# Kernel optimization log

Hardware: AMD Instinct MI355X
Metric: run time of the kernel (lower is better)

## Reference

```python
import jax, jax.numpy as jnp
import numpy as np

V, E, H, TAG, L = 50000, 256, 256, 20, 2
T = TAG + 2  # +START/STOP
START, STOP = TAG, TAG + 1
B, S = 128, 256
EPS = 1e-5


def _lstm_dir(x, w_ih, w_hh, b_ih, b_hh, reverse):
    # x: [B,S,in]; w_ih: [4H,in]; w_hh: [4H,H]
    xg = jnp.einsum('bsi,gi->bsg', x, w_ih) + b_ih  # [B,S,4H]
    Hd = w_hh.shape[-1]
    def step(carry, xt):
        h, c = carry
        g = xt + h @ w_hh.T + b_hh
        i, f, gg, o = jnp.split(g, 4, axis=-1)  # torch gate order i,f,g,o
        c = jax.nn.sigmoid(f) * c + jax.nn.sigmoid(i) * jnp.tanh(gg)
        h = jax.nn.sigmoid(o) * jnp.tanh(c)
        return (h, c), h
    init = (jnp.zeros((x.shape[0], Hd), x.dtype), jnp.zeros((x.shape[0], Hd), x.dtype))
    _, hs = jax.lax.scan(step, init, xg.transpose(1, 0, 2), reverse=reverse)
    return hs.transpose(1, 0, 2)


def _bilstm_layer(x, w_ih, w_hh, b_ih, b_hh):
    fwd = _lstm_dir(x, w_ih[0], w_hh[0], b_ih[0], b_hh[0], False)
    bwd = _lstm_dir(x, w_ih[1], w_hh[1], b_ih[1], b_hh[1], True)
    return jnp.concatenate([fwd, bwd], axis=-1)


def _crf_nll(feats, mask, tags, trans):
    # feats: [B,S,T]; trans[from,to]; mask: [B,S] int
    Bn, Sn, Tn = feats.shape
    m = mask.astype(feats.dtype)
    # --- log partition via forward algorithm ---
    alpha = trans[START][None, :] + feats[:, 0]  # [B,T]
    def step(alpha, inp):
        emit, mt = inp  # [B,T], [B]
        new = jax.nn.logsumexp(alpha[:, :, None] + trans[None, :, :], axis=1) + emit
        return jnp.where(mt[:, None] > 0, new, alpha), None
    alpha, _ = jax.lax.scan(step, alpha, (feats[:, 1:].transpose(1, 0, 2), mask[:, 1:].T))
    logZ = jax.nn.logsumexp(alpha + trans[:, STOP][None, :], axis=1)  # [B]
    # --- gold path score ---
    emit = jnp.take_along_axis(feats, tags[:, :, None], axis=2)[:, :, 0]  # [B,S]
    emit_score = (emit * m).sum(axis=1)
    tr_score = trans[START, tags[:, 0]]
    tr_score = tr_score + (trans[tags[:, :-1], tags[:, 1:]] * m[:, 1:]).sum(axis=1)
    last_idx = (mask.sum(axis=1) - 1).astype(jnp.int32)
    last_tag = jnp.take_along_axis(tags, last_idx[:, None].astype(tags.dtype), axis=1)[:, 0]
    tr_score = tr_score + trans[last_tag, STOP]
    return jnp.mean(logZ - emit_score - tr_score)


def _forward(embedding, w_ih0, w_hh0, b_ih0, b_hh0, w_ih1, w_hh1, b_ih1, b_hh1,
             ln_g, ln_b, w_out, b_out, trans, word_input, mask, tags):
    x = embedding[word_input]  # [B,S,E] (dropout off at eval)
    x = _bilstm_layer(x, w_ih0, w_hh0, b_ih0, b_hh0)  # [B,S,2H]
    x = _bilstm_layer(x, w_ih1, w_hh1, b_ih1, b_hh1)  # [B,S,2H]
    mu = x.mean(axis=-1, keepdims=True)
    var = ((x - mu) ** 2).mean(axis=-1, keepdims=True)
    x = (x - mu) * jax.lax.rsqrt(var + EPS) * ln_g + ln_b
    feats = jnp.einsum('bsh,th->bst', x, w_out) + b_out  # [B,S,T]
    return _crf_nll(feats, mask, tags, trans)


def setup_inputs() -> dict:
    key = jax.random.key(0)
    ks = jax.random.split(key, 20)
    sc = 0.05
    inp = {
        'embedding': jax.random.uniform(ks[0], (V, E), jnp.float32, -0.1, 0.1),
        'w_ih0': jax.random.normal(ks[1], (2, 4 * H, E), jnp.float32) * sc,
        'w_hh0': jax.random.normal(ks[2], (2, 4 * H, H), jnp.float32) * sc,
        'b_ih0': jnp.zeros((2, 4 * H), jnp.float32),
        'b_hh0': jnp.zeros((2, 4 * H), jnp.float32),
        'w_ih1': jax.random.normal(ks[3], (2, 4 * H, 2 * H), jnp.float32) * sc,
        'w_hh1': jax.random.normal(ks[4], (2, 4 * H, H), jnp.float32) * sc,
        'b_ih1': jnp.zeros((2, 4 * H), jnp.float32),
        'b_hh1': jnp.zeros((2, 4 * H), jnp.float32),
        'ln_g': jnp.ones((2 * H,), jnp.float32),
        'ln_b': jnp.zeros((2 * H,), jnp.float32),
        'w_out': jax.random.normal(ks[5], (T, 2 * H), jnp.float32) * sc,
        'b_out': jnp.zeros((T,), jnp.float32),
        'trans': jax.random.normal(ks[6], (T, T), jnp.float32) * sc,
        'word_input': jax.random.randint(ks[7], (B, S), 0, V, jnp.int64),
        'mask': jnp.ones((B, S), jnp.int32),
        'tags': jax.random.randint(ks[8], (B, S), 0, TAG, jnp.int64),
    }
    return inp


def reference(embedding, w_ih0, w_hh0, b_ih0, b_hh0, w_ih1, w_hh1, b_ih1, b_hh1,
              ln_g, ln_b, w_out, b_out, trans, word_input, mask, tags):
    return _forward(embedding, w_ih0, w_hh0, b_ih0, b_hh0, w_ih1, w_hh1, b_ih1, b_hh1,
                    ln_g, ln_b, w_out, b_out, trans, word_input, mask, tags)
```

## Files before the change

kernel.cpp:

```cpp
#include <hip/hip_runtime.h>
#include <stdint.h>

#define DEVINL __device__ __forceinline__

typedef __attribute__((ext_vector_type(8))) __bf16 bf16x8;
typedef __attribute__((ext_vector_type(8))) unsigned short ushort8;
typedef __attribute__((ext_vector_type(4))) float floatx4;

constexpr int E_ = 256;
constexpr int TAGS = 22, ST_START = 20, ST_STOP = 21;
constexpr int B_ = 128, S_ = 256, BS_ = B_ * S_;
constexpr int NG = 1024;

DEVINL uint16_t f2bf(float f) {
  uint32_t u = __builtin_bit_cast(uint32_t, f);
  return (uint16_t)((u + 0x7fffu + ((u >> 16) & 1u)) >> 16);
}
DEVINL float bf2f(uint16_t h) {
  uint32_t u = ((uint32_t)h) << 16;
  return __builtin_bit_cast(float, u);
}
DEVINL uint4 pack8(float4 a, float4 b) {
  ushort8 h;
  h[0] = f2bf(a.x); h[1] = f2bf(a.y); h[2] = f2bf(a.z); h[3] = f2bf(a.w);
  h[4] = f2bf(b.x); h[5] = f2bf(b.y); h[6] = f2bf(b.z); h[7] = f2bf(b.w);
  return __builtin_bit_cast(uint4, h);
}
DEVINL floatx4 mfma16(uint4 a, uint4 b, floatx4 c) {
  return __builtin_amdgcn_mfma_f32_16x16x32_bf16(
      __builtin_bit_cast(bf16x8, a), __builtin_bit_cast(bf16x8, b), c, 0, 0, 0);
}
DEVINL float sigf(float x) { return 1.f / (1.f + __expf(-x)); }
DEVINL float tanh_(float x) { return 1.f - 2.f / (__expf(2.f * x) + 1.f); }

__global__ void k_init(float* out, int out_n) {
  int t = threadIdx.x;
  if (t < out_n) out[t] = 0.f;
}

__global__ void k_f2bf(const float* __restrict__ src, uint16_t* __restrict__ dst, int n) {
  int i = blockIdx.x * blockDim.x + threadIdx.x;
  int stride = gridDim.x * blockDim.x;
  for (; i < n; i += stride) dst[i] = f2bf(src[i]);
}

template <bool EMBED, int K>
__global__ __launch_bounds__(256) void k_gemm(
    const float* __restrict__ emb, const int* __restrict__ word,
    const uint16_t* __restrict__ xa, const uint16_t* __restrict__ wb,
    uint16_t* __restrict__ xg) {
  __shared__ uint4 As[8 * 128];
  __shared__ uint4 Bs[8 * 128];
  const int tid = threadIdx.x;
  const int bx = blockIdx.x;
  const int m0 = (bx & 255) << 7;
  const int n0 = (bx >> 8) << 7;
  const int lane = tid & 63, w = tid >> 6;
  const int ln = lane & 15, q = lane >> 4;
  const int wm = w & 1, wn = w >> 1;

  floatx4 acc[4][4];
#pragma unroll
  for (int a = 0; a < 4; a++)
#pragma unroll
    for (int b = 0; b < 4; b++) acc[a][b] = (floatx4){0.f, 0.f, 0.f, 0.f};

  for (int k0 = 0; k0 < K; k0 += 64) {
#pragma unroll
    for (int it = 0; it < 4; it++) {
      int c = tid + it * 256;
      int k8 = c & 7, r = c >> 3;
      if (EMBED) {
        int row = word[m0 + r];
        const float* sp = emb + (size_t)row * E_ + k0 + k8 * 8;
        float4 f0 = *(const float4*)sp;
        float4 f1 = *(const float4*)(sp + 4);
        As[k8 * 128 + r] = pack8(f0, f1);
      } else {
        As[k8 * 128 + r] = *(const uint4*)(xa + (size_t)(m0 + r) * K + k0 + k8 * 8);
      }
      Bs[k8 * 128 + r] = *(const uint4*)(wb + (size_t)(n0 + r) * K + k0 + k8 * 8);
    }
    __syncthreads();
#pragma unroll
    for (int kk = 0; kk < 2; kk++) {
      const int k4b = kk * 4 + q;
      uint4 af[4], bf[4];
#pragma unroll
      for (int mt = 0; mt < 4; mt++) af[mt] = As[k4b * 128 + wm * 64 + mt * 16 + ln];
#pragma unroll
      for (int nt = 0; nt < 4; nt++) bf[nt] = Bs[k4b * 128 + wn * 64 + nt * 16 + ln];
#pragma unroll
      for (int mt = 0; mt < 4; mt++)
#pragma unroll
        for (int nt = 0; nt < 4; nt++) acc[mt][nt] = mfma16(af[mt], bf[nt], acc[mt][nt]);
    }
    __syncthreads();
  }
#pragma unroll
  for (int mt = 0; mt < 4; mt++) {
    int Rb = m0 + wm * 64 + mt * 16 + q * 4;
#pragma unroll
    for (int nt = 0; nt < 4; nt++) {
      int C = n0 + wn * 64 + nt * 16 + ln;
      size_t base = (size_t)(C >> 10) * ((size_t)BS_ * NG) + (C & 1023);
#pragma unroll
      for (int r = 0; r < 4; r++) xg[base + (size_t)(Rb + r) * NG] = f2bf(acc[mt][nt][r]);
    }
  }
}

__global__ __launch_bounds__(256) void k_rec(
    const uint16_t* __restrict__ xg, const float* __restrict__ w_hh,
    const float* __restrict__ b_ih, const float* __restrict__ b_hh,
    uint16_t* __restrict__ xout, uint64_t* __restrict__ hbuf, int ebase) {
  __shared__ uint4 Wl[32 * 64];
  __shared__ uint32_t hA32[4096];
  __shared__ float gates[32 * 66];
  __shared__ uint32_t xstage[16 * 256];
  __shared__ float bias_s[64];

  const int tid = threadIdx.x;
  const int wg = blockIdx.x;
  const int group = wg & 7, member = wg >> 3;
  const int dir = group & 1, tile = group >> 1;
  const int j0 = member * 16;
  const int lane = tid & 63, w = tid >> 6, ln = lane & 15, q = lane >> 4;

  for (int p = tid; p < 2048; p += 256) {
    int n = p & 63, k4 = p >> 6;
    int row = dir * 1024 + (n >> 4) * 256 + j0 + (n & 15);
    const float* sp = w_hh + (size_t)row * 256 + k4 * 8;
    float4 f0 = *(const float4*)sp;
    float4 f1 = *(const float4*)(sp + 4);
    Wl[k4 * 64 + n] = pack8(f0, f1);
  }
  if (tid < 64) {
    int row = dir * 1024 + (tid >> 4) * 256 + j0 + (tid & 15);
    bias_s[tid] = b_ih[row] + b_hh[row];
  }
  __syncthreads();

  const int nloc = w * 16 + ln;
  const int nglob = w * 256 + j0 + ln;
  const float breg = bias_s[nloc];
  const uint16_t* xgd = xg + (size_t)dir * BS_ * NG;

  const int msr = tid & 31, jp = tid >> 5;
  const int cp = member * 8 + jp;
  const int e_pub = (cp >> 2) * 128 + msr * 4 + (cp & 3);
  float c0 = 0.f, c1 = 0.f;

  const int xr0 = tile * 32 + q * 4;
  int sg = dir ? 255 : 0;
  uint16_t xv[8];
#pragma unroll
  for (int r = 0; r < 4; r++) {
    xv[r] = xgd[(size_t)((xr0 + r) * 256 + sg) * NG + nglob];
    xv[4 + r] = xgd[(size_t)((xr0 + 16 + r) * 256 + sg) * NG + nglob];
  }

  const uint4* hAv = (const uint4*)hA32;

  for (int t = 0; t < 256; t++) {
    sg = dir ? (255 - t) : t;
    floatx4 acc0 = (floatx4){0.f, 0.f, 0.f, 0.f};
    floatx4 acc1 = (floatx4){0.f, 0.f, 0.f, 0.f};
    if (t > 0) {
      const uint64_t* hsrc = hbuf + (size_t)((((t - 1) & 1) * 8) + group) * 4096;
      const uint32_t want = (uint32_t)(ebase + t);
      uint64_t v[16];
      while (true) {
#pragma unroll
        for (int i = 0; i < 16; i++)
          v[i] = __hip_atomic_load(&hsrc[tid + 256 * i], __ATOMIC_RELAXED,
                                   __HIP_MEMORY_SCOPE_AGENT);
        bool fresh = true;
#pragma unroll
        for (int i = 0; i < 16; i++) fresh &= ((uint32_t)(v[i] >> 32) == want);
        if (fresh) break;
        __builtin_amdgcn_s_sleep(1);
      }
#pragma unroll
      for (int i = 0; i < 16; i++) hA32[tid + 256 * i] = (uint32_t)v[i];
      __syncthreads();
#pragma unroll
      for (int kk = 0; kk < 8; kk++) {
        int k4b = kk * 4 + q;
        uint4 bfr = Wl[k4b * 64 + nloc];
        acc0 = mfma16(hAv[k4b * 32 + ln], bfr, acc0);
        acc1 = mfma16(hAv[k4b * 32 + 16 + ln], bfr, acc1);
      }
    }
#pragma unroll
    for (int r = 0; r < 4; r++) {
      gates[(q * 4 + r) * 66 + nloc] = acc0[r] + bf2f(xv[r]) + breg;
      gates[(16 + q * 4 + r) * 66 + nloc] = acc1[r] + bf2f(xv[4 + r]) + breg;
    }
    {
      int tn = (t < 255) ? (t + 1) : 255;
      int sgn = dir ? (255 - tn) : tn;
#pragma unroll
      for (int r = 0; r < 4; r++) {
        xv[r] = xgd[(size_t)((xr0 + r) * 256 + sgn) * NG + nglob];
        xv[4 + r] = xgd[(size_t)((xr0 + 16 + r) * 256 + sgn) * NG + nglob];
      }
    }
    __syncthreads();
    const float* gr = gates + msr * 66 + 2 * jp;
    float ig0 = gr[0], fg0 = gr[16], gg0 = gr[32], og0 = gr[48];
    float ig1 = gr[1], fg1 = gr[17], gg1 = gr[33], og1 = gr[49];
    c0 = sigf(fg0) * c0 + sigf(ig0) * tanh_(gg0);
    c1 = sigf(fg1) * c1 + sigf(ig1) * tanh_(gg1);
    float h0 = sigf(og0) * tanh_(c0);
    float h1 = sigf(og1) * tanh_(c1);
    uint32_t hpack = (uint32_t)f2bf(h0) | ((uint32_t)f2bf(h1) << 16);
    xstage[(t & 15) * 256 + jp * 32 + msr] = hpack;
    if (t < 255) {
      uint64_t pk = (uint64_t)hpack | ((uint64_t)(uint32_t)(ebase + t + 1) << 32);
      __hip_atomic_store(&hbuf[(size_t)(((t & 1) * 8) + group) * 4096 + e_pub], pk,
                         __ATOMIC_RELAXED, __HIP_MEMORY_SCOPE_AGENT);
    }
    if ((t & 15) == 15) {
      __syncthreads();
#pragma unroll
      for (int pp = 0; pp < 2; pp++) {
        int p = tid + pp * 256;
        int m = p & 31, u = p >> 5;
        int tt = t - 15 + u;
        int ssg = dir ? (255 - tt) : tt;
        uint32_t d[8];
#pragma unroll
        for (int jj = 0; jj < 8; jj++) d[jj] = xstage[u * 256 + jj * 32 + m];
        uint16_t* dst = xout + ((size_t)(tile * 32 + m) * 256 + ssg) * 512 + dir * 256 + j0;
        ((uint4*)dst)[0] = (uint4){d[0], d[1], d[2], d[3]};
        ((uint4*)dst)[1] = (uint4){d[4], d[5], d[6], d[7]};
      }
    }
  }
}

__global__ __launch_bounds__(256) void k_lnproj(
    const uint16_t* __restrict__ x2, const float* __restrict__ ln_g,
    const float* __restrict__ ln_b, const float* __restrict__ w_out,
    const float* __restrict__ b_out, float* __restrict__ feats) {
  const int w = threadIdx.x >> 6, lane = threadIdx.x & 63;
  const int row = blockIdx.x * 4 + w;
  ushort8 xu = __builtin_bit_cast(ushort8, *((const uint4*)(x2 + (size_t)row * 512) + lane));
  float f[8];
  float s = 0.f, ss = 0.f;
#pragma unroll
  for (int j = 0; j < 8; j++) {
    f[j] = bf2f(xu[j]);
    s += f[j];
    ss += f[j] * f[j];
  }
#pragma unroll
  for (int o = 1; o < 64; o <<= 1) {
    s += __shfl_xor(s, o, 64);
    ss += __shfl_xor(ss, o, 64);
  }
  float mu = s * (1.f / 512.f);
  float var = ss * (1.f / 512.f) - mu * mu;
  float rs = rsqrtf(var + 1e-5f);
  const float4 g0 = *(const float4*)(ln_g + lane * 8);
  const float4 g1 = *(const float4*)(ln_g + lane * 8 + 4);
  const float4 bb0 = *(const float4*)(ln_b + lane * 8);
  const float4 bb1 = *(const float4*)(ln_b + lane * 8 + 4);
  float gl[8] = {g0.x, g0.y, g0.z, g0.w, g1.x, g1.y, g1.z, g1.w};
  float bl[8] = {bb0.x, bb0.y, bb0.z, bb0.w, bb1.x, bb1.y, bb1.z, bb1.w};
  float xh[8];
#pragma unroll
  for (int j = 0; j < 8; j++) xh[j] = (f[j] - mu) * rs * gl[j] + bl[j];
  float* fr = feats + (size_t)row * TAGS;
  for (int tg = 0; tg < TAGS; tg++) {
    const float4 w0 = *(const float4*)(w_out + tg * 512 + lane * 8);
    const float4 w1 = *(const float4*)(w_out + tg * 512 + lane * 8 + 4);
    float p = xh[0] * w0.x + xh[1] * w0.y + xh[2] * w0.z + xh[3] * w0.w + xh[4] * w1.x +
              xh[5] * w1.y + xh[6] * w1.z + xh[7] * w1.w;
#pragma unroll
    for (int o = 1; o < 64; o <<= 1) p += __shfl_xor(p, o, 64);
    if (lane == 0) fr[tg] = p + b_out[tg];
  }
}

__global__ __launch_bounds__(64) void k_crf(
    const float* __restrict__ feats, const float* __restrict__ trans,
    const int* __restrict__ mask, const int* __restrict__ tags, float* __restrict__ out) {
  const int b = blockIdx.x, j = threadIdx.x;
  const bool act = j < TAGS;
  float tcol[TAGS];
#pragma unroll
  for (int i = 0; i < TAGS; i++) tcol[i] = act ? trans[i * TAGS + j] : 0.f;
  const float tstop = act ? trans[j * TAGS + ST_STOP] : 0.f;
  const float* fb = feats + (size_t)b * 256 * TAGS;
  const int* mb = mask + b * 256;
  const int* tb = tags + b * 256;
  float alpha = act ? (tcol[ST_START] + fb[j]) : -1e30f;
  for (int t = 1; t < 256; t++) {
    float vv[TAGS];
    float mx = -1e30f;
#pragma unroll
    for (int i = 0; i < TAGS; i++) {
      float v = __shfl(alpha, i, 64) + tcol[i];
      vv[i] = v;
      mx = fmaxf(mx, v);
    }
    float s = 0.f;
#pragma unroll
    for (int i = 0; i < TAGS; i++) s += __expf(vv[i] - mx);
    float nw = mx + __logf(s) + (act ? fb[t * TAGS + j] : 0.f);
    if (act && mb[t] > 0) alpha = nw;
  }
  float z = act ? (alpha + tstop) : -1e30f;
  float mz = z;
#pragma unroll
  for (int o = 1; o < 64; o <<= 1) mz = fmaxf(mz, __shfl_xor(mz, o, 64));
  float se = act ? __expf(z - mz) : 0.f;
#pragma unroll
  for (int o = 1; o < 64; o <<= 1) se += __shfl_xor(se, o, 64);
  float logZ = mz + __logf(se);
  float em = 0.f;
  int cnt = 0;
  for (int tt = j; tt < 256; tt += 64) {
    int m = mb[tt];
    cnt += m;
    if (m > 0) em += fb[tt * TAGS + tb[tt]];
  }
#pragma unroll
  for (int o = 1; o < 64; o <<= 1) {
    em += __shfl_xor(em, o, 64);
    cnt += __shfl_xor(cnt, o, 64);
  }
  float tr = 0.f;
  for (int tt = 1 + j; tt < 256; tt += 64)
    if (mb[tt] > 0) tr += trans[tb[tt - 1] * TAGS + tb[tt]];
#pragma unroll
  for (int o = 1; o < 64; o <<= 1) tr += __shfl_xor(tr, o, 64);
  if (j == 0) {
    tr += trans[ST_START * TAGS + tb[0]];
    int last = cnt - 1;
    tr += trans[tb[last] * TAGS + ST_STOP];
    atomicAdd(out, (logZ - em - tr) * (1.f / 128.f));
  }
}

extern "C" void kernel_launch(void* const* d_in, const int* in_sizes, int n_in, void* d_out,
                              int out_size, void* d_ws, size_t ws_size, hipStream_t stream) {
  (void)in_sizes;
  (void)n_in;
  const float* emb = (const float*)d_in[0];
  const float* w_ih0 = (const float*)d_in[1];
  const float* w_hh0 = (const float*)d_in[2];
  const float* b_ih0 = (const float*)d_in[3];
  const float* b_hh0 = (const float*)d_in[4];
  const float* w_ih1 = (const float*)d_in[5];
  const float* w_hh1 = (const float*)d_in[6];
  const float* b_ih1 = (const float*)d_in[7];
  const float* b_hh1 = (const float*)d_in[8];
  const float* ln_g = (const float*)d_in[9];
  const float* ln_b = (const float*)d_in[10];
  const float* w_out = (const float*)d_in[11];
  const float* b_out = (const float*)d_in[12];
  const float* trans = (const float*)d_in[13];
  const int* word = (const int*)d_in[14];
  const int* mask = (const int*)d_in[15];
  const int* tags = (const int*)d_in[16];

  char* ws = (char*)d_ws;
  size_t off = 0;
  auto take = [&](size_t bytes) -> char* {
    char* p = ws + off;
    off = (off + bytes + 255) & ~(size_t)255;
    return p;
  };
  uint16_t* wb0 = (uint16_t*)take((size_t)2048 * 256 * 2);
  uint16_t* wb1 = (uint16_t*)take((size_t)2048 * 512 * 2);
  uint16_t* xg = (uint16_t*)take((size_t)2 * BS_ * 1024 * 2);
  uint16_t* x1 = (uint16_t*)take((size_t)BS_ * 512 * 2);
  float* feats = (float*)take((size_t)BS_ * TAGS * 4);
  uint64_t* hbuf = (uint64_t*)take((size_t)2 * 8 * 4096 * 8);
  if (off > ws_size) return;
  float* out = (float*)d_out;

  hipLaunchKernelGGL(k_init, dim3(1), dim3(256), 0, stream, out, out_size);
  hipLaunchKernelGGL(k_f2bf, dim3(512), dim3(256), 0, stream, w_ih0, wb0, 2048 * 256);
  hipLaunchKernelGGL(k_f2bf, dim3(512), dim3(256), 0, stream, w_ih1, wb1, 2048 * 512);
  hipLaunchKernelGGL((k_gemm<true, 256>), dim3(4096), dim3(256), 0, stream, emb, word,
                     (const uint16_t*)nullptr, wb0, xg);
  hipLaunchKernelGGL(k_rec, dim3(128), dim3(256), 0, stream, xg, w_hh0, b_ih0, b_hh0, x1, hbuf,
                     0);
  hipLaunchKernelGGL((k_gemm<false, 512>), dim3(4096), dim3(256), 0, stream,
                     (const float*)nullptr, (const int*)nullptr, x1, wb1, xg);
  hipLaunchKernelGGL(k_rec, dim3(128), dim3(256), 0, stream, xg, w_hh1, b_ih1, b_hh1, x1, hbuf,
                     256);
  hipLaunchKernelGGL(k_lnproj, dim3(8192), dim3(256), 0, stream, x1, ln_g, ln_b, w_out, b_out,
                     feats);
  hipLaunchKernelGGL(k_crf, dim3(128), dim3(64), 0, stream, feats, trans, mask, tags, out);
}
```

Baseline: 1.671 ms.

## Halve recurrent workgroups, keep W_hh in registers, fuse gate math in-lane

The recurrent LSTM kernel now runs 64 workgroups that each own 32 hidden units instead of 128 owning 16. The W_hh slice is preloaded into registers, so the per-step MFMA loop no longer reads weights from LDS. Each lane computes all four gates for its own rows, which removes the gates LDS round-trip and one barrier per step. The h exchange buffer is double-buffered and output staging is flushed every 8 steps. The trade-off is fewer workgroups doing twice the work per step, much higher register pressure, and a longer spin-wait sleep.

```diff
diff --git a/kernel.cpp b/kernel.cpp
--- a/kernel.cpp
+++ b/kernel.cpp
@@ -110,62 +110,64 @@
   }
 }
 
-__global__ __launch_bounds__(256) void k_rec(
+__global__ __launch_bounds__(256, 1) void k_rec(
     const uint16_t* __restrict__ xg, const float* __restrict__ w_hh,
     const float* __restrict__ b_ih, const float* __restrict__ b_hh,
     uint16_t* __restrict__ xout, uint64_t* __restrict__ hbuf, int ebase) {
-  __shared__ uint4 Wl[32 * 64];
-  __shared__ uint32_t hA32[4096];
-  __shared__ float gates[32 * 66];
-  __shared__ uint32_t xstage[16 * 256];
-  __shared__ float bias_s[64];
+  __shared__ uint4 Wl[32 * 128];
+  __shared__ uint32_t hA32[2 * 4096];
+  __shared__ uint32_t xstage[8 * 512];
 
   const int tid = threadIdx.x;
   const int wg = blockIdx.x;
   const int group = wg & 7, member = wg >> 3;
   const int dir = group & 1, tile = group >> 1;
-  const int j0 = member * 16;
+  const int j0m = member * 32;
   const int lane = tid & 63, w = tid >> 6, ln = lane & 15, q = lane >> 4;
-
-  for (int p = tid; p < 2048; p += 256) {
-    int n = p & 63, k4 = p >> 6;
-    int row = dir * 1024 + (n >> 4) * 256 + j0 + (n & 15);
+  const int mh = w >> 1, jh = w & 1;
+
+  for (int p = tid; p < 4096; p += 256) {
+    int nloc = p & 127, k4 = p >> 7;
+    int g = (nloc >> 4) & 3, jj = (nloc >> 6) * 16 + (nloc & 15);
+    int row = dir * 1024 + g * 256 + j0m + jj;
     const float* sp = w_hh + (size_t)row * 256 + k4 * 8;
-    float4 f0 = *(const float4*)sp;
-    float4 f1 = *(const float4*)(sp + 4);
-    Wl[k4 * 64 + n] = pack8(f0, f1);
-  }
-  if (tid < 64) {
-    int row = dir * 1024 + (tid >> 4) * 256 + j0 + (tid & 15);
-    bias_s[tid] = b_ih[row] + b_hh[row];
-  }
+    Wl[k4 * 128 + nloc] = pack8(*(const float4*)sp, *(const float4*)(sp + 4));
+  }
+  const int j = j0m + jh * 16 + ln;
+  float brg[4];
+#pragma unroll
+  for (int g = 0; g < 4; g++) brg[g] = b_ih[dir * 1024 + g * 256 + j] +
+                                       b_hh[dir * 1024 + g * 256 + j];
   __syncthreads();
 
-  const int nloc = w * 16 + ln;
-  const int nglob = w * 256 + j0 + ln;
-  const float breg = bias_s[nloc];
+  uint4 Wb[8][4];
+#pragma unroll
+  for (int kk = 0; kk < 8; kk++)
+#pragma unroll
+    for (int g = 0; g < 4; g++)
+      Wb[kk][g] = Wl[(kk * 4 + q) * 128 + jh * 64 + g * 16 + ln];
+
   const uint16_t* xgd = xg + (size_t)dir * BS_ * NG;
-
-  const int msr = tid & 31, jp = tid >> 5;
-  const int cp = member * 8 + jp;
-  const int e_pub = (cp >> 2) * 128 + msr * 4 + (cp & 3);
-  float c0 = 0.f, c1 = 0.f;
-
-  const int xr0 = tile * 32 + q * 4;
+  const int mbase = mh * 16 + q * 4;
+  const int mrow0 = tile * 32 + mbase;
+  const bool even = (ln & 1) == 0;
+  const int jp = j >> 1;
+  const int jpl = jh * 8 + (ln >> 1);
+
+  float c[4] = {0.f, 0.f, 0.f, 0.f};
+  uint16_t xv[16];
   int sg = dir ? 255 : 0;
-  uint16_t xv[8];
-#pragma unroll
-  for (int r = 0; r < 4; r++) {
-    xv[r] = xgd[(size_t)((xr0 + r) * 256 + sg) * NG + nglob];
-    xv[4 + r] = xgd[(size_t)((xr0 + 16 + r) * 256 + sg) * NG + nglob];
-  }
-
-  const uint4* hAv = (const uint4*)hA32;
+#pragma unroll
+  for (int g = 0; g < 4; g++)
+#pragma unroll
+    for (int r = 0; r < 4; r++)
+      xv[g * 4 + r] = xgd[(size_t)((mrow0 + r) * 256 + sg) * NG + g * 256 + j];
 
   for (int t = 0; t < 256; t++) {
     sg = dir ? (255 - t) : t;
-    floatx4 acc0 = (floatx4){0.f, 0.f, 0.f, 0.f};
-    floatx4 acc1 = (floatx4){0.f, 0.f, 0.f, 0.f};
+    floatx4 acc[4];
+#pragma unroll
+    for (int g = 0; g < 4; g++) acc[g] = (floatx4){0.f, 0.f, 0.f, 0.f};
     if (t > 0) {
       const uint64_t* hsrc = hbuf + (size_t)((((t - 1) & 1) * 8) + group) * 4096;
       const uint32_t want = (uint32_t)(ebase + t);
@@ -179,63 +181,73 @@
 #pragma unroll
         for (int i = 0; i < 16; i++) fresh &= ((uint32_t)(v[i] >> 32) == want);
         if (fresh) break;
-        __builtin_amdgcn_s_sleep(1);
+        __builtin_amdgcn_s_sleep(2);
       }
-#pragma unroll
-      for (int i = 0; i < 16; i++) hA32[tid + 256 * i] = (uint32_t)v[i];
+      uint32_t* hAw = hA32 + (t & 1) * 4096;
+#pragma unroll
+      for (int i = 0; i < 16; i++) hAw[tid + 256 * i] = (uint32_t)v[i];
       __syncthreads();
+      const uint4* hAv = (const uint4*)(hA32 + (t & 1) * 4096);
 #pragma unroll
       for (int kk = 0; kk < 8; kk++) {
-        int k4b = kk * 4 + q;
-        uint4 bfr = Wl[k4b * 64 + nloc];
-        acc0 = mfma16(hAv[k4b * 32 + ln], bfr, acc0);
-        acc1 = mfma16(hAv[k4b * 32 + 16 + ln], bfr, acc1);
+        uint4 a = hAv[(kk * 4 + q) * 32 + mh * 16 + ln];
+#pragma unroll
+        for (int g = 0; g < 4; g++) acc[g] = mfma16(a, Wb[kk][g], acc[g]);
       }
     }
+    float hr[4];
 #pragma unroll
     for (int r = 0; r < 4; r++) {
-      gates[(q * 4 + r) * 66 + nloc] = acc0[r] + bf2f(xv[r]) + breg;
-      gates[(16 + q * 4 + r) * 66 + nloc] = acc1[r] + bf2f(xv[4 + r]) + breg;
+      float pi = acc[0][r] + bf2f(xv[0 + r]) + brg[0];
+      float pf = acc[1][r] + bf2f(xv[4 + r]) + brg[1];
+      float pg = acc[2][r] + bf2f(xv[8 + r]) + brg[2];
+      float po = acc[3][r] + bf2f(xv[12 + r]) + brg[3];
+      c[r] = sigf(pf) * c[r] + sigf(pi) * tanh_(pg);
+      hr[r] = sigf(po) * tanh_(c[r]);
+    }
+    uint32_t hp[4];
+#pragma unroll
+    for (int r = 0; r < 4; r++) {
+      float hn = __shfl_xor(hr[r], 1);
+      hp[r] = (uint32_t)f2bf(hr[r]) | ((uint32_t)f2bf(hn) << 16);
+    }
+    if (even && t < 255) {
+      uint64_t* hdst = hbuf + (size_t)(((t & 1) * 8) + group) * 4096;
+      const uint64_t ep = ((uint64_t)(uint32_t)(ebase + t + 1)) << 32;
+#pragma unroll
+      for (int r = 0; r < 4; r++) {
+        int e = (jp >> 2) * 128 + (mbase + r) * 4 + (jp & 3);
+        __hip_atomic_store(&hdst[e], ep | (uint64_t)hp[r], __ATOMIC_RELAXED,
+                           __HIP_MEMORY_SCOPE_AGENT);
+      }
     }
     {
-      int tn = (t < 255) ? (t + 1) : 255;
+      int tn = (t < 255) ? t + 1 : 255;
       int sgn = dir ? (255 - tn) : tn;
 #pragma unroll
-      for (int r = 0; r < 4; r++) {
-        xv[r] = xgd[(size_t)((xr0 + r) * 256 + sgn) * NG + nglob];
-        xv[4 + r] = xgd[(size_t)((xr0 + 16 + r) * 256 + sgn) * NG + nglob];
-      }
-    }
-    __syncthreads();
-    const float* gr = gates + msr * 66 + 2 * jp;
-    float ig0 = gr[0], fg0 = gr[16], gg0 = gr[32], og0 = gr[48];
-    float ig1 = gr[1], fg1 = gr[17], gg1 = gr[33], og1 = gr[49];
-    c0 = sigf(fg0) * c0 + sigf(ig0) * tanh_(gg0);
-    c1 = sigf(fg1) * c1 + sigf(ig1) * tanh_(gg1);
-    float h0 = sigf(og0) * tanh_(c0);
-    float h1 = sigf(og1) * tanh_(c1);
-    uint32_t hpack = (uint32_t)f2bf(h0) | ((uint32_t)f2bf(h1) << 16);
-    xstage[(t & 15) * 256 + jp * 32 + msr] = hpack;
-    if (t < 255) {
-      uint64_t pk = (uint64_t)hpack | ((uint64_t)(uint32_t)(ebase + t + 1) << 32);
-      __hip_atomic_store(&hbuf[(size_t)(((t & 1) * 8) + group) * 4096 + e_pub], pk,
-                         __ATOMIC_RELAXED, __HIP_MEMORY_SCOPE_AGENT);
-    }
-    if ((t & 15) == 15) {
+      for (int g = 0; g < 4; g++)
+#pragma unroll
+        for (int r = 0; r < 4; r++)
+          xv[g * 4 + r] = xgd[(size_t)((mrow0 + r) * 256 + sgn) * NG + g * 256 + j];
+    }
+    if (even) {
+#pragma unroll
+      for (int r = 0; r < 4; r++)
+        xstage[(t & 7) * 512 + jpl * 32 + mbase + r] = hp[r];
+    }
+    if ((t & 7) == 7) {
       __syncthreads();
-#pragma unroll
-      for (int pp = 0; pp < 2; pp++) {
-        int p = tid + pp * 256;
-        int m = p & 31, u = p >> 5;
-        int tt = t - 15 + u;
-        int ssg = dir ? (255 - tt) : tt;
-        uint32_t d[8];
-#pragma unroll
-        for (int jj = 0; jj < 8; jj++) d[jj] = xstage[u * 256 + jj * 32 + m];
-        uint16_t* dst = xout + ((size_t)(tile * 32 + m) * 256 + ssg) * 512 + dir * 256 + j0;
-        ((uint4*)dst)[0] = (uint4){d[0], d[1], d[2], d[3]};
-        ((uint4*)dst)[1] = (uint4){d[4], d[5], d[6], d[7]};
-      }
+      int m = tid & 31, u = tid >> 5;
+      int tt = t - 7 + u;
+      int ssg = dir ? (255 - tt) : tt;
+      uint32_t d[16];
+#pragma unroll
+      for (int k = 0; k < 16; k++) d[k] = xstage[u * 512 + k * 32 + m];
+      uint16_t* dst = xout + ((size_t)(tile * 32 + m) * 256 + ssg) * 512 + dir * 256 + j0m;
+      ((uint4*)dst)[0] = (uint4){d[0], d[1], d[2], d[3]};
+      ((uint4*)dst)[1] = (uint4){d[4], d[5], d[6], d[7]};
+      ((uint4*)dst)[2] = (uint4){d[8], d[9], d[10], d[11]};
+      ((uint4*)dst)[3] = (uint4){d[12], d[13], d[14], d[15]};
     }
   }
 }
@@ -388,11 +400,11 @@
   hipLaunchKernelGGL(k_f2bf, dim3(512), dim3(256), 0, stream, w_ih1, wb1, 2048 * 512);
   hipLaunchKernelGGL((k_gemm<true, 256>), dim3(4096), dim3(256), 0, stream, emb, word,
                      (const uint16_t*)nullptr, wb0, xg);
-  hipLaunchKernelGGL(k_rec, dim3(128), dim3(256), 0, stream, xg, w_hh0, b_ih0, b_hh0, x1, hbuf,
+  hipLaunchKernelGGL(k_rec, dim3(64), dim3(256), 0, stream, xg, w_hh0, b_ih0, b_hh0, x1, hbuf,
                      0);
   hipLaunchKernelGGL((k_gemm<false, 512>), dim3(4096), dim3(256), 0, stream,
                      (const float*)nullptr, (const int*)nullptr, x1, wb1, xg);
-  hipLaunchKernelGGL(k_rec, dim3(128), dim3(256), 0, stream, xg, w_hh1, b_ih1, b_hh1, x1, hbuf,
+  hipLaunchKernelGGL(k_rec, dim3(64), dim3(256), 0, stream, xg, w_hh1, b_ih1, b_hh1, x1, hbuf,
                      256);
   hipLaunchKernelGGL(k_lnproj, dim3(8192), dim3(256), 0, stream, x1, ln_g, ln_b, w_out, b_out,
                      feats);
```

Measured after the change: 1.943 ms. 16.2% more time.

## Negotiate same-XCC groups to use workgroup-scope atomics for hidden-state exchange

Applied to the files above, without the earlier changes.

Each recurrent workgroup publishes its XCC id, and when all 16 members of a direction/tile group sit on the same XCC, the per-step hidden-state exchange uses workgroup-scope atomic loads and stores instead of agent-scope ones. The intent is to keep these exchanges in the shared per-XCC L2 and cut cross-die coherence latency on the sequential critical path. A periodic agent-scope reload is kept as a fallback. The next-step xg prefetch is also moved after the h publish and output writeback so the publish is issued earlier. The fast path relies on workgroup scope being visible across CUs in one L2, which is not guaranteed by the memory model, and it is only taken when block placement happens to put a whole group on one XCC.

```diff
diff --git a/kernel.cpp b/kernel.cpp
--- a/kernel.cpp
+++ b/kernel.cpp
@@ -119,6 +119,7 @@
   __shared__ float gates[32 * 66];
   __shared__ uint32_t xstage[16 * 256];
   __shared__ float bias_s[64];
+  __shared__ int negf;
 
   const int tid = threadIdx.x;
   const int wg = blockIdx.x;
@@ -126,6 +127,15 @@
   const int dir = group & 1, tile = group >> 1;
   const int j0 = member * 16;
   const int lane = tid & 63, w = tid >> 6, ln = lane & 15, q = lane >> 4;
+
+  uint32_t xcc;
+  asm volatile("s_getreg_b32 %0, hwreg(HW_REG_XCC_ID, 0, 32)" : "=s"(xcc));
+  xcc &= 7u;
+  uint64_t* nego = hbuf + 65536;
+  const uint32_t wantn = 0x5AFE0000u + (uint32_t)ebase;
+  if (tid == 0)
+    __hip_atomic_store(&nego[group * 16 + member], (((uint64_t)wantn) << 32) | xcc,
+                       __ATOMIC_RELAXED, __HIP_MEMORY_SCOPE_AGENT);
 
   for (int p = tid; p < 2048; p += 256) {
     int n = p & 63, k4 = p >> 6;
@@ -139,7 +149,21 @@
     int row = dir * 1024 + (tid >> 4) * 256 + j0 + (tid & 15);
     bias_s[tid] = b_ih[row] + b_hh[row];
   }
+  if (tid < 64) {
+    bool ok = true;
+    if (tid < 16) {
+      uint64_t v;
+      do {
+        v = __hip_atomic_load(&nego[group * 16 + tid], __ATOMIC_RELAXED,
+                              __HIP_MEMORY_SCOPE_AGENT);
+      } while ((uint32_t)(v >> 32) != wantn);
+      ok = ((uint32_t)v == xcc);
+    }
+    unsigned long long bal = __ballot(ok);
+    if (tid == 0) negf = (bal == 0xFFFFFFFFFFFFFFFFull) ? 1 : 0;
+  }
   __syncthreads();
+  const bool l2fast = (negf != 0);
 
   const int nloc = w * 16 + ln;
   const int nglob = w * 256 + j0 + ln;
@@ -170,15 +194,24 @@
       const uint64_t* hsrc = hbuf + (size_t)((((t - 1) & 1) * 8) + group) * 4096;
       const uint32_t want = (uint32_t)(ebase + t);
       uint64_t v[16];
+      int rounds = 0;
       while (true) {
-#pragma unroll
-        for (int i = 0; i < 16; i++)
-          v[i] = __hip_atomic_load(&hsrc[tid + 256 * i], __ATOMIC_RELAXED,
-                                   __HIP_MEMORY_SCOPE_AGENT);
+        if (l2fast && ((rounds & 3) != 3)) {
+#pragma unroll
+          for (int i = 0; i < 16; i++)
+            v[i] = __hip_atomic_load(&hsrc[tid + 256 * i], __ATOMIC_RELAXED,
+                                     __HIP_MEMORY_SCOPE_WORKGROUP);
+        } else {
+#pragma unroll
+          for (int i = 0; i < 16; i++)
+            v[i] = __hip_atomic_load(&hsrc[tid + 256 * i], __ATOMIC_RELAXED,
+                                     __HIP_MEMORY_SCOPE_AGENT);
+        }
         bool fresh = true;
 #pragma unroll
         for (int i = 0; i < 16; i++) fresh &= ((uint32_t)(v[i] >> 32) == want);
         if (fresh) break;
+        rounds++;
         __builtin_amdgcn_s_sleep(1);
       }
 #pragma unroll
@@ -196,15 +229,6 @@
     for (int r = 0; r < 4; r++) {
       gates[(q * 4 + r) * 66 + nloc] = acc0[r] + bf2f(xv[r]) + breg;
       gates[(16 + q * 4 + r) * 66 + nloc] = acc1[r] + bf2f(xv[4 + r]) + breg;
-    }
-    {
-      int tn = (t < 255) ? (t + 1) : 255;
-      int sgn = dir ? (255 - tn) : tn;
-#pragma unroll
-      for (int r = 0; r < 4; r++) {
-        xv[r] = xgd[(size_t)((xr0 + r) * 256 + sgn) * NG + nglob];
-        xv[4 + r] = xgd[(size_t)((xr0 + 16 + r) * 256 + sgn) * NG + nglob];
-      }
     }
     __syncthreads();
     const float* gr = gates + msr * 66 + 2 * jp;
@@ -215,12 +239,15 @@
     float h0 = sigf(og0) * tanh_(c0);
     float h1 = sigf(og1) * tanh_(c1);
     uint32_t hpack = (uint32_t)f2bf(h0) | ((uint32_t)f2bf(h1) << 16);
-    xstage[(t & 15) * 256 + jp * 32 + msr] = hpack;
     if (t < 255) {
       uint64_t pk = (uint64_t)hpack | ((uint64_t)(uint32_t)(ebase + t + 1) << 32);
-      __hip_atomic_store(&hbuf[(size_t)(((t & 1) * 8) + group) * 4096 + e_pub], pk,
-                         __ATOMIC_RELAXED, __HIP_MEMORY_SCOPE_AGENT);
-    }
+      uint64_t* hdst = &hbuf[(size_t)(((t & 1) * 8) + group) * 4096 + e_pub];
+      if (l2fast)
+        __hip_atomic_store(hdst, pk, __ATOMIC_RELAXED, __HIP_MEMORY_SCOPE_WORKGROUP);
+      else
+        __hip_atomic_store(hdst, pk, __ATOMIC_RELAXED, __HIP_MEMORY_SCOPE_AGENT);
+    }
+    xstage[(t & 15) * 256 + jp * 32 + msr] = hpack;
     if ((t & 15) == 15) {
       __syncthreads();
 #pragma unroll
@@ -235,6 +262,15 @@
         uint16_t* dst = xout + ((size_t)(tile * 32 + m) * 256 + ssg) * 512 + dir * 256 + j0;
         ((uint4*)dst)[0] = (uint4){d[0], d[1], d[2], d[3]};
         ((uint4*)dst)[1] = (uint4){d[4], d[5], d[6], d[7]};
+      }
+    }
+    {
+      int tn = (t < 255) ? (t + 1) : 255;
+      int sgn = dir ? (255 - tn) : tn;
+#pragma unroll
+      for (int r = 0; r < 4; r++) {
+        xv[r] = xgd[(size_t)((xr0 + r) * 256 + sgn) * NG + nglob];
+        xv[4 + r] = xgd[(size_t)((xr0 + 16 + r) * 256 + sgn) * NG + nglob];
       }
     }
   }
@@ -379,7 +415,7 @@
   uint16_t* xg = (uint16_t*)take((size_t)2 * BS_ * 1024 * 2);
   uint16_t* x1 = (uint16_t*)take((size_t)BS_ * 512 * 2);
   float* feats = (float*)take((size_t)BS_ * TAGS * 4);
-  uint64_t* hbuf = (uint64_t*)take((size_t)2 * 8 * 4096 * 8);
+  uint64_t* hbuf = (uint64_t*)take(((size_t)2 * 8 * 4096 + 256) * 8);
   if (off > ws_size) return;
   float* out = (float*)d_out;
 
```

Result: slower. 1.797 ms (+7.5%).
